# Performance work log

Measured on AMD Instinct MI355X. Metric: run time of the kernel, lower is better.

The kernel has to match this reference:

```python
import jax, jax.numpy as jnp
import numpy as np

N_NODES = 524288
N_EDGES = 786432
NUM_GRAPHS = 8192
NUM_NODE_TYPES = 16
NODE_DIM = 256
EDGE_DIM = 128
OUT_DIM = 1


def setup_inputs() -> dict:
    key = jax.random.key(0)
    ks = jax.random.split(key, 12)
    h_node = jax.random.uniform(ks[0], (N_NODES, NUM_NODE_TYPES), dtype=jnp.float32)
    pos_node = jax.random.normal(ks[1], (N_NODES, 3), dtype=jnp.float32)
    batch_node = jnp.sort(jax.random.randint(ks[2], (N_NODES,), 0, NUM_GRAPHS)).astype(jnp.int64)
    edge_index = jax.random.randint(ks[3], (2, N_EDGES), 0, N_NODES).astype(jnp.int64)
    batch_edge = jnp.sort(jax.random.randint(ks[4], (N_EDGES,), 0, NUM_GRAPHS)).astype(jnp.int64)
    s = 0.05
    W_node = jax.random.normal(ks[5], (NUM_NODE_TYPES, NODE_DIM), dtype=jnp.float32) * s
    W_edge = jax.random.normal(ks[6], (2 * NUM_NODE_TYPES, EDGE_DIM), dtype=jnp.float32) * s
    H = NODE_DIM + EDGE_DIM
    W1 = jax.random.normal(ks[7], (H, H), dtype=jnp.float32) * s
    b1 = jnp.zeros((H,), dtype=jnp.float32)
    W2 = jax.random.normal(ks[8], (H, OUT_DIM), dtype=jnp.float32) * s
    b2 = jnp.zeros((OUT_DIM,), dtype=jnp.float32)
    return {"h_node": h_node, "pos_node": pos_node, "batch_node": batch_node,
            "edge_index": edge_index, "batch_edge": batch_edge,
            "W_node": W_node, "W_edge": W_edge, "W1": W1, "b1": b1, "W2": W2, "b2": b2}


def _segment_mean(x, seg_ids, num_segments):
    # fused replacement for the original per-graph boolean-mask loop:
    # h[seg==k].mean(0) for all k, via one scatter-add + count normalize
    sums = jax.ops.segment_sum(x, seg_ids, num_segments=num_segments)
    cnts = jax.ops.segment_sum(jnp.ones((x.shape[0],), x.dtype), seg_ids, num_segments=num_segments)
    return sums / jnp.maximum(cnts, 1.0)[:, None]


def reference(h_node, pos_node, batch_node, edge_index, batch_edge,
              W_node, W_edge, W1, b1, W2, b2):
    # h_edge = cat(h_node[src], h_node[dst])  -> [E, 2*num_node_types]
    h_edge_raw = jnp.concatenate([h_node[edge_index[0]], h_node[edge_index[1]]], axis=-1)
    # num_timesteps == 0 path: plain embedders, no time embedding
    hn = h_node @ W_node          # [N, node_dim]
    he = h_edge_raw @ W_edge      # [E, edge_dim]
    # encoder treated as identity (NodeEdgeNet not in scope); pooling is the target op
    node_mean = _segment_mean(hn, batch_node, NUM_GRAPHS)  # [G, node_dim]
    edge_mean = _segment_mean(he, batch_edge, NUM_GRAPHS)  # [G, edge_dim]
    h_sub = jnp.concatenate([node_mean, edge_mean], axis=-1)  # [G, node_dim+edge_dim]
    # final MLP (num_layer=2): Linear -> ReLU -> Linear
    pred = jax.nn.relu(h_sub @ W1 + b1) @ W2 + b2  # [G, 1]
    return pred
```

## Files before the change

kernel.cpp:

```cpp
#include <hip/hip_runtime.h>

#define N_NODES_C   524288
#define N_EDGES_C   786432
#define NUM_GRAPHS_C 8192
#define NT 16
#define NODE_DIM_C 256
#define EDGE_DIM_C 128
#define HDIM 384
#define KC 48

#define FOLD_BLOCKS  72
#define MEAN_BLOCKS  4096
#define TOTAL_BLOCKS (FOLD_BLOCKS + MEAN_BLOCKS)

#define WS_NM    0
#define WS_EM    524288
#define WS_WC    1572864

__device__ __forceinline__ int lower_bound_i32(const int* __restrict__ a, int n, int key) {
    int lo = 0, hi = n;
    while (lo < hi) {
        int mid = (lo + hi) >> 1;
        if (a[mid] < key) lo = mid + 1; else hi = mid;
    }
    return lo;
}

__device__ __forceinline__ void wave_seg_bounds(const int* __restrict__ b, int n,
                                                int g, int lane, int& s, int& e) {
    int key = g + ((lane >= 32) ? 1 : 0);
    int lo = lower_bound_i32(b, n, key);
    s = __shfl(lo, 0, 64);
    e = __shfl(lo, 32, 64);
}

__device__ __forceinline__ void f4_add(float4& a, const float4 v) {
    a.x += v.x; a.y += v.y; a.z += v.z; a.w += v.w;
}

__device__ __forceinline__ void f4_shfl_xor_add(float4& a, int mask) {
    a.x += __shfl_xor(a.x, mask, 64);
    a.y += __shfl_xor(a.y, mask, 64);
    a.z += __shfl_xor(a.z, mask, 64);
    a.w += __shfl_xor(a.w, mask, 64);
}

__global__ __launch_bounds__(256) void km_mega(
    const float* __restrict__ h_node,
    const int* __restrict__ bnode, const int* __restrict__ bedge,
    const int* __restrict__ esrc, const int* __restrict__ edst,
    const float* __restrict__ Wn, const float* __restrict__ We,
    const float* __restrict__ W1,
    float* __restrict__ nm, float* __restrict__ em, float* __restrict__ Wc) {
    int blk  = blockIdx.x;
    int wave = threadIdx.x >> 6;
    int lane = threadIdx.x & 63;
    const float4* h4 = (const float4*)h_node;

    if (blk < FOLD_BLOCKS) {
        int o = blk * 256 + threadIdx.x;
        if (o >= KC * HDIM) return;
        int k = o / HDIM, j = o % HDIM;
        float acc = 0.f;
        if (k < NT) {
            const float* wr = &Wn[k * NODE_DIM_C];
            #pragma unroll 16
            for (int kk = 0; kk < NODE_DIM_C; ++kk)
                acc = fmaf(wr[kk], W1[(size_t)kk * HDIM + j], acc);
        } else {
            const float* wr = &We[(k - NT) * EDGE_DIM_C];
            #pragma unroll 16
            for (int kk = 0; kk < EDGE_DIM_C; ++kk)
                acc = fmaf(wr[kk], W1[(size_t)(NODE_DIM_C + kk) * HDIM + j], acc);
        }
        Wc[o] = acc;
        return;
    }

    int t  = blk - FOLD_BLOCKS;
    int gb = t >> 1;

    if ((t & 1) == 0) {
        int g = gb * 4 + wave;
        int s, e;
        wave_seg_bounds(bedge, N_EDGES_C, g, lane, s, e);
        int eo   = lane >> 3;
        int p    = (lane >> 2) & 1;
        int quad = lane & 3;
        const int* __restrict__ idxp = p ? edst : esrc;
        float4 a0 = make_float4(0.f, 0.f, 0.f, 0.f);
        float4 a1 = a0, a2 = a0, a3 = a0;
        int base = s + (eo << 2);
        for (int i = base; i < e; i += 32) {
            int v0 = idxp[i];
            float4 r0 = h4[(size_t)v0 * 4 + quad];
            f4_add(a0, r0);
            if (i + 1 < e) {
                int v1 = idxp[i + 1];
                f4_add(a1, h4[(size_t)v1 * 4 + quad]);
            }
            if (i + 2 < e) {
                int v2 = idxp[i + 2];
                f4_add(a2, h4[(size_t)v2 * 4 + quad]);
            }
            if (i + 3 < e) {
                int v3 = idxp[i + 3];
                f4_add(a3, h4[(size_t)v3 * 4 + quad]);
            }
        }
        f4_add(a0, a1); f4_add(a2, a3); f4_add(a0, a2);
        f4_shfl_xor_add(a0, 8);
        f4_shfl_xor_add(a0, 16);
        f4_shfl_xor_add(a0, 32);
        if (eo == 0) {
            float inv = 1.f / fmaxf((float)(e - s), 1.f);
            ((float4*)em)[(size_t)g * 8 + p * 4 + quad] =
                make_float4(a0.x * inv, a0.y * inv, a0.z * inv, a0.w * inv);
        }
    } else {
        int g = gb * 4 + wave;
        int s, e;
        wave_seg_bounds(bnode, N_NODES_C, g, lane, s, e);
        int row_off = lane >> 2;
        int quad    = lane & 3;
        float4 a0 = make_float4(0.f, 0.f, 0.f, 0.f);
        float4 a1 = a0;
        int i = s + row_off;
        for (; i + 16 < e; i += 32) {
            float4 v0 = h4[(size_t)i * 4 + quad];
            float4 v1 = h4[(size_t)(i + 16) * 4 + quad];
            f4_add(a0, v0);
            f4_add(a1, v1);
        }
        if (i < e) f4_add(a0, h4[(size_t)i * 4 + quad]);
        f4_add(a0, a1);
        f4_shfl_xor_add(a0, 4);
        f4_shfl_xor_add(a0, 8);
        f4_shfl_xor_add(a0, 16);
        f4_shfl_xor_add(a0, 32);
        if (row_off == 0) {
            float inv = 1.f / fmaxf((float)(e - s), 1.f);
            ((float4*)nm)[(size_t)g * 4 + quad] =
                make_float4(a0.x * inv, a0.y * inv, a0.z * inv, a0.w * inv);
        }
    }
}

#define GPB 16
__global__ __launch_bounds__(HDIM) void k3_mlp(
    const float* __restrict__ nm, const float* __restrict__ em,
    const float* __restrict__ Wc, const float* __restrict__ b1,
    const float* __restrict__ W2, const float* __restrict__ b2,
    float* __restrict__ pred) {
    int j = threadIdx.x;
    float wc[KC];
    #pragma unroll
    for (int k = 0; k < KC; ++k) wc[k] = Wc[k * HDIM + j];
    float b1j = b1[j], w2j = W2[j], b20 = b2[0];

    __shared__ float fs[GPB][KC];
    __shared__ float part[GPB][6];
    int g0 = blockIdx.x * GPB;
    #pragma unroll
    for (int t = j; t < GPB * KC; t += HDIM) {
        int g = t / KC, k = t % KC;
        fs[g][k] = (k < NT) ? nm[(size_t)(g0 + g) * NT + k]
                            : em[(size_t)(g0 + g) * 32 + (k - NT)];
    }
    __syncthreads();

    int wave = j >> 6, lane = j & 63;
    for (int g = 0; g < GPB; ++g) {
        float z = b1j;
        #pragma unroll
        for (int k = 0; k < KC; ++k) z = fmaf(fs[g][k], wc[k], z);
        z = fmaxf(z, 0.f);
        float p = z * w2j;
        #pragma unroll
        for (int off = 32; off > 0; off >>= 1) p += __shfl_down(p, off, 64);
        if (lane == 0) part[g][wave] = p;
    }
    __syncthreads();
    if (j < GPB) {
        float sacc = b20;
        #pragma unroll
        for (int w = 0; w < 6; ++w) sacc += part[j][w];
        pred[g0 + j] = sacc;
    }
}

extern "C" void kernel_launch(void* const* d_in, const int* in_sizes, int n_in,
                              void* d_out, int out_size, void* d_ws, size_t ws_size,
                              hipStream_t stream) {
    const float* h_node     = (const float*)d_in[0];
    const int*   batch_node = (const int*)d_in[2];
    const int*   edge_index = (const int*)d_in[3];
    const int*   batch_edge = (const int*)d_in[4];
    const float* W_node     = (const float*)d_in[5];
    const float* W_edge     = (const float*)d_in[6];
    const float* W1         = (const float*)d_in[7];
    const float* b1         = (const float*)d_in[8];
    const float* W2         = (const float*)d_in[9];
    const float* b2         = (const float*)d_in[10];
    float* pred = (float*)d_out;

    char* ws = (char*)d_ws;
    float* nm = (float*)(ws + WS_NM);
    float* em = (float*)(ws + WS_EM);
    float* Wc = (float*)(ws + WS_WC);

    const int* esrc = edge_index;
    const int* edst = edge_index + N_EDGES_C;

    km_mega<<<TOTAL_BLOCKS, 256, 0, stream>>>(
        h_node, batch_node, batch_edge, esrc, edst, W_node, W_edge, W1, nm, em, Wc);
    k3_mlp<<<NUM_GRAPHS_C / GPB, HDIM, 0, stream>>>(nm, em, Wc, b1, W2, b2, pred);
}
```

Measured before the change: 166.4 us.

## Vectorize edge index loads with int4 prefetch and reorder block roles

The edge-mean path now reads source/destination indices as aligned int4 groups and prefetches the next group one iteration ahead, so the gathers do not wait on scalar index loads. Partial groups at segment boundaries fall back to per-element masked adds. Block assignment changes from interleaved fold/edge/node blocks to contiguous node blocks, then edge blocks, then fold blocks. This adds boundary-handling branches and alters how the block scheduler mixes streaming and gather work.

```diff
diff --git a/kernel.cpp b/kernel.cpp
--- a/kernel.cpp
+++ b/kernel.cpp
@@ -9,9 +9,12 @@
 #define HDIM 384
 #define KC 48
 
+#define NODE_BLOCKS  2048
+#define EDGE_BLOCKS  2048
 #define FOLD_BLOCKS  72
-#define MEAN_BLOCKS  4096
-#define TOTAL_BLOCKS (FOLD_BLOCKS + MEAN_BLOCKS)
+#define EDGE_BASE    NODE_BLOCKS
+#define FOLD_BASE    (NODE_BLOCKS + EDGE_BLOCKS)
+#define TOTAL_BLOCKS (NODE_BLOCKS + EDGE_BLOCKS + FOLD_BLOCKS)
 
 #define WS_NM    0
 #define WS_EM    524288
@@ -57,8 +60,76 @@
     int lane = threadIdx.x & 63;
     const float4* h4 = (const float4*)h_node;
 
-    if (blk < FOLD_BLOCKS) {
-        int o = blk * 256 + threadIdx.x;
+    if (blk < NODE_BLOCKS) {
+        int g = blk * 4 + wave;
+        int s, e;
+        wave_seg_bounds(bnode, N_NODES_C, g, lane, s, e);
+        int row_off = lane >> 2;
+        int quad    = lane & 3;
+        float4 a0 = make_float4(0.f, 0.f, 0.f, 0.f);
+        float4 a1 = a0;
+        int i = s + row_off;
+        for (; i + 16 < e; i += 32) {
+            float4 v0 = h4[(size_t)i * 4 + quad];
+            float4 v1 = h4[(size_t)(i + 16) * 4 + quad];
+            f4_add(a0, v0);
+            f4_add(a1, v1);
+        }
+        if (i < e) f4_add(a0, h4[(size_t)i * 4 + quad]);
+        f4_add(a0, a1);
+        f4_shfl_xor_add(a0, 4);
+        f4_shfl_xor_add(a0, 8);
+        f4_shfl_xor_add(a0, 16);
+        f4_shfl_xor_add(a0, 32);
+        if (row_off == 0) {
+            float inv = 1.f / fmaxf((float)(e - s), 1.f);
+            ((float4*)nm)[(size_t)g * 4 + quad] =
+                make_float4(a0.x * inv, a0.y * inv, a0.z * inv, a0.w * inv);
+        }
+    } else if (blk < FOLD_BASE) {
+        int g = (blk - EDGE_BASE) * 4 + wave;
+        int s, e;
+        wave_seg_bounds(bedge, N_EDGES_C, g, lane, s, e);
+        int eo   = lane >> 3;
+        int p    = (lane >> 2) & 1;
+        int quad = lane & 3;
+        const int*  __restrict__ idxp  = p ? edst : esrc;
+        const int4* __restrict__ idx4p = (const int4*)idxp;
+        float4 a0 = make_float4(0.f, 0.f, 0.f, 0.f);
+        float4 a1 = a0, a2 = a0, a3 = a0;
+        int G0 = s >> 2;
+        int G1 = (e - 1) >> 2;
+        int G  = G0 + eo;
+        int4 nx = (G <= G1) ? idx4p[G] : make_int4(0, 0, 0, 0);
+        while (G <= G1) {
+            int4 cur = nx;
+            int base = G << 2;
+            int Gn = G + 8;
+            if (Gn <= G1) nx = idx4p[Gn];
+            if (base >= s && base + 3 < e) {
+                f4_add(a0, h4[(size_t)cur.x * 4 + quad]);
+                f4_add(a1, h4[(size_t)cur.y * 4 + quad]);
+                f4_add(a2, h4[(size_t)cur.z * 4 + quad]);
+                f4_add(a3, h4[(size_t)cur.w * 4 + quad]);
+            } else {
+                if (base     >= s && base     < e) f4_add(a0, h4[(size_t)cur.x * 4 + quad]);
+                if (base + 1 >= s && base + 1 < e) f4_add(a1, h4[(size_t)cur.y * 4 + quad]);
+                if (base + 2 >= s && base + 2 < e) f4_add(a2, h4[(size_t)cur.z * 4 + quad]);
+                if (base + 3 >= s && base + 3 < e) f4_add(a3, h4[(size_t)cur.w * 4 + quad]);
+            }
+            G = Gn;
+        }
+        f4_add(a0, a1); f4_add(a2, a3); f4_add(a0, a2);
+        f4_shfl_xor_add(a0, 8);
+        f4_shfl_xor_add(a0, 16);
+        f4_shfl_xor_add(a0, 32);
+        if (eo == 0) {
+            float inv = 1.f / fmaxf((float)(e - s), 1.f);
+            ((float4*)em)[(size_t)g * 8 + p * 4 + quad] =
+                make_float4(a0.x * inv, a0.y * inv, a0.z * inv, a0.w * inv);
+        }
+    } else {
+        int o = (blk - FOLD_BASE) * 256 + threadIdx.x;
         if (o >= KC * HDIM) return;
         int k = o / HDIM, j = o % HDIM;
         float acc = 0.f;
@@ -74,75 +145,6 @@
                 acc = fmaf(wr[kk], W1[(size_t)(NODE_DIM_C + kk) * HDIM + j], acc);
         }
         Wc[o] = acc;
-        return;
-    }
-
-    int t  = blk - FOLD_BLOCKS;
-    int gb = t >> 1;
-
-    if ((t & 1) == 0) {
-        int g = gb * 4 + wave;
-        int s, e;
-        wave_seg_bounds(bedge, N_EDGES_C, g, lane, s, e);
-        int eo   = lane >> 3;
-        int p    = (lane >> 2) & 1;
-        int quad = lane & 3;
-        const int* __restrict__ idxp = p ? edst : esrc;
-        float4 a0 = make_float4(0.f, 0.f, 0.f, 0.f);
-        float4 a1 = a0, a2 = a0, a3 = a0;
-        int base = s + (eo << 2);
-        for (int i = base; i < e; i += 32) {
-            int v0 = idxp[i];
-            float4 r0 = h4[(size_t)v0 * 4 + quad];
-            f4_add(a0, r0);
-            if (i + 1 < e) {
-                int v1 = idxp[i + 1];
-                f4_add(a1, h4[(size_t)v1 * 4 + quad]);
-            }
-            if (i + 2 < e) {
-                int v2 = idxp[i + 2];
-                f4_add(a2, h4[(size_t)v2 * 4 + quad]);
-            }
-            if (i + 3 < e) {
-                int v3 = idxp[i + 3];
-                f4_add(a3, h4[(size_t)v3 * 4 + quad]);
-            }
-        }
-        f4_add(a0, a1); f4_add(a2, a3); f4_add(a0, a2);
-        f4_shfl_xor_add(a0, 8);
-        f4_shfl_xor_add(a0, 16);
-        f4_shfl_xor_add(a0, 32);
-        if (eo == 0) {
-            float inv = 1.f / fmaxf((float)(e - s), 1.f);
-            ((float4*)em)[(size_t)g * 8 + p * 4 + quad] =
-                make_float4(a0.x * inv, a0.y * inv, a0.z * inv, a0.w * inv);
-        }
-    } else {
-        int g = gb * 4 + wave;
-        int s, e;
-        wave_seg_bounds(bnode, N_NODES_C, g, lane, s, e);
-        int row_off = lane >> 2;
-        int quad    = lane & 3;
-        float4 a0 = make_float4(0.f, 0.f, 0.f, 0.f);
-        float4 a1 = a0;
-        int i = s + row_off;
-        for (; i + 16 < e; i += 32) {
-            float4 v0 = h4[(size_t)i * 4 + quad];
-            float4 v1 = h4[(size_t)(i + 16) * 4 + quad];
-            f4_add(a0, v0);
-            f4_add(a1, v1);
-        }
-        if (i < e) f4_add(a0, h4[(size_t)i * 4 + quad]);
-        f4_add(a0, a1);
-        f4_shfl_xor_add(a0, 4);
-        f4_shfl_xor_add(a0, 8);
-        f4_shfl_xor_add(a0, 16);
-        f4_shfl_xor_add(a0, 32);
-        if (row_off == 0) {
-            float inv = 1.f / fmaxf((float)(e - s), 1.f);
-            ((float4*)nm)[(size_t)g * 4 + quad] =
-                make_float4(a0.x * inv, a0.y * inv, a0.z * inv, a0.w * inv);
-        }
     }
 }
 
```

After: 152.7 us. -8.2%, faster.
